# Kernel optimization log

Hardware: AMD Instinct MI355X
Metric: run time of the kernel (lower is better)

Reference implementation:

```python
import jax, jax.numpy as jnp
import numpy as np


def _chamfer(pred, target):
    # pred: [B, N, 3], target: [B, M, 3]
    # Squared euclidean pairwise distances (norm=2 in pytorch3d semantics):
    # d[b,n,m] = |p|^2 + |t|^2 - 2 p.t
    p2 = jnp.sum(pred * pred, axis=-1)      # [B, N]
    t2 = jnp.sum(target * target, axis=-1)  # [B, M]
    pt = jnp.einsum('bnd,bmd->bnm', pred, target)  # [B, N, M]
    d = p2[:, :, None] + t2[:, None, :] - 2.0 * pt  # [B, N, M]
    # bidirectional nearest-neighbor min-reduction
    cham_x = jnp.min(d, axis=2)  # [B, N] pred -> target
    cham_y = jnp.min(d, axis=1)  # [B, M] target -> pred
    # point_reduction='mean' then batch_reduction='mean' (pytorch3d defaults)
    loss = jnp.mean(jnp.mean(cham_x, axis=1) + jnp.mean(cham_y, axis=1))
    return loss


def setup_inputs() -> dict:
    key = jax.random.key(0)
    k1, k2 = jax.random.split(key)
    B, N, M, D = 16, 4096, 4096, 3
    pred = jax.random.normal(k1, (B, N, D), dtype=jnp.float32)
    target = jax.random.normal(k2, (B, M, D), dtype=jnp.float32)
    return {"pred": pred, "target": target}


def reference(pred, target):
    return _chamfer(pred, target)
```

## Files before the change

kernel.cpp:

```cpp
#include <hip/hip_runtime.h>

typedef __attribute__((ext_vector_type(8)))  short short8;
typedef __attribute__((ext_vector_type(16))) float f32x16;

#define B_SZ  16
#define NPTS  4096
#define MBLK  512
#define PRB   256
#define NCH   (NPTS / PRB)
#define STGT  512
#define STILE (STGT / 32)
#define NSTG  (NPTS / STGT)
#define NRT   (B_SZ * NPTS)

__device__ __forceinline__ unsigned short f2bf(float f) {
    unsigned u = __float_as_uint(f);
    return (unsigned short)((u + 0x7FFFu + ((u >> 16) & 1u)) >> 16);
}
__device__ __forceinline__ float bf2f(unsigned short s) {
    return __uint_as_float(((unsigned)s) << 16);
}
__device__ __forceinline__ short n2(unsigned short s) {
    return (short)f2bf(-2.0f * bf2f(s));
}

__global__ __launch_bounds__(MBLK, 2) void chamfer_fused(
    const float* __restrict__ pred, const float* __restrict__ target,
    float* __restrict__ out)
{
    __shared__ short8   sB[STILE * 64];
    __shared__ unsigned rowOut[PRB];
    __shared__ float    red[MBLK / 64];

    const int dir = blockIdx.y;
    const float* own = dir ? target : pred;
    const float* opp = dir ? pred : target;

    const int b     = blockIdx.x >> 4;
    const int chunk = blockIdx.x & (NCH - 1);
    const int tid   = threadIdx.x;
    const int lane  = tid & 63;
    const int w     = tid >> 6;
    const int r32   = lane & 31;
    const int h     = lane >> 5;
    const short ONE = (short)0x3F80;

    short8 af;
    {
        const float* pp = own +
            ((size_t)b*NPTS + chunk*PRB + w*32 + r32)*3;
        float x = pp[0], y = pp[1], z = pp[2];
        unsigned short phx=f2bf(x), phy=f2bf(y), phz=f2bf(z);
        unsigned short plx=f2bf(x-bf2f(phx)), ply=f2bf(y-bf2f(phy)),
                       plz=f2bf(z-bf2f(phz));
        short8 v;
        if (h == 0) {
            v[0]=n2(phx); v[1]=n2(phy); v[2]=n2(phz);
            v[3]=n2(plx); v[4]=n2(ply); v[5]=n2(plz);
            v[6]=n2(phx); v[7]=n2(phy);
        } else {
            float p2 = fmaf(z,z,fmaf(y,y,x*x));
            unsigned short p2h=f2bf(p2), p2l=f2bf(p2-bf2f(p2h));
            v[0]=n2(phz); v[1]=n2(plx); v[2]=n2(ply); v[3]=n2(plz);
            v[4]=(short)p2h; v[5]=(short)p2l; v[6]=ONE; v[7]=ONE;
        }
        af = v;
    }

    f32x16 zc;
    #pragma unroll
    for (int r = 0; r < 16; ++r) zc[r] = 0.0f;
    short8 mA = {0,0,0,0,0,0,0,0}, mB = {0,0,0,0,0,0,0,0};
    if (h == 0) { mA[0] = (short)f2bf((float)r32); mB[0] = ONE; }
    f32x16 pr = __builtin_amdgcn_mfma_f32_32x32x16_bf16(mA, mB, zc, 0, 0, 0);
    int lab[16];
    bool ok = true;
    #pragma unroll
    for (int r = 0; r < 16; ++r) {
        lab[r] = ((int)(pr[r] + 0.5f)) & 31;
        ok = ok && (lab[r] == ((r & 3) + 8 * (r >> 2) + 4 * h));
    }
    const bool fast = __all(ok) != 0;

    if (!fast) rowOut[tid & (PRB - 1)] = 0x7F7F7F7Fu;

    f32x16 rmin;
    #pragma unroll
    for (int r = 0; r < 16; ++r) rmin[r] = 1e30f;

    const float* oppB = opp + (size_t)b * NPTS * 3;

    for (int s = 0; s < NSTG; ++s) {
        __syncthreads();
        #pragma unroll
        for (int i = 0; i < (STILE*64)/MBLK; ++i) {
            int e  = i * MBLK + tid;
            int t  = e >> 6, l2 = e & 63;
            int cc = l2 & 31, hh = l2 >> 5;
            const float* o = oppB + (size_t)(s*STGT + t*32 + cc)*3;
            float tx=o[0], ty=o[1], tz=o[2];
            unsigned short hx=f2bf(tx), hy=f2bf(ty), hz=f2bf(tz);
            unsigned short lx=f2bf(tx-bf2f(hx)), ly=f2bf(ty-bf2f(hy)),
                           lz=f2bf(tz-bf2f(hz));
            short8 v;
            if (hh == 0) {
                v[0]=(short)hx; v[1]=(short)hy; v[2]=(short)hz;
                v[3]=(short)hx; v[4]=(short)hy; v[5]=(short)hz;
                v[6]=(short)lx; v[7]=(short)ly;
            } else {
                float t2 = fmaf(tz,tz,fmaf(ty,ty,tx*tx));
                unsigned short t2h=f2bf(t2), t2l=f2bf(t2-bf2f(t2h));
                v[0]=(short)lz; v[1]=(short)lx; v[2]=(short)ly;
                v[3]=(short)lz; v[4]=ONE; v[5]=ONE;
                v[6]=(short)t2h; v[7]=(short)t2l;
            }
            sB[e] = v;
        }
        __syncthreads();

        for (int t = 0; t < STILE; ++t) {
            short8 b0 = sB[t*64 + lane];
            f32x16 a0 = __builtin_amdgcn_mfma_f32_32x32x16_bf16(af, b0, zc, 0,0,0);
            #pragma unroll
            for (int r = 0; r < 16; ++r)
                rmin[r] = fminf(a0[r], rmin[r]);
        }
    }

    __syncthreads();
    if (fast) {
        #pragma unroll
        for (int r = 0; r < 16; ++r) {
            float v0 = rmin[r];
            v0 = fminf(v0, __shfl_xor(v0, 1, 64));
            v0 = fminf(v0, __shfl_xor(v0, 2, 64));
            v0 = fminf(v0, __shfl_xor(v0, 4, 64));
            v0 = fminf(v0, __shfl_xor(v0, 8, 64));
            v0 = fminf(v0, __shfl_xor(v0, 16, 64));
            if (r32 == 0)
                rowOut[w*32 + lab[r]] = __float_as_uint(v0);
        }
    } else {
        #pragma unroll
        for (int r = 0; r < 16; ++r)
            atomicMin(&rowOut[w*32 + lab[r]],
                      __float_as_uint(fmaxf(rmin[r], 0.0f)));
    }
    __syncthreads();

    float v = (tid < PRB) ? __uint_as_float(rowOut[tid]) : 0.0f;
    for (int off = 32; off > 0; off >>= 1)
        v += __shfl_down(v, off, 64);
    if ((tid & 63) == 0) red[w] = v;
    __syncthreads();
    if (tid == 0) {
        float s = 0.0f;
        #pragma unroll
        for (int i = 0; i < MBLK / 64; ++i) s += red[i];
        atomicAdd(out, s * (1.0f / (float)NRT));
    }
}

extern "C" void kernel_launch(void* const* d_in, const int* in_sizes, int n_in,
                              void* d_out, int out_size, void* d_ws, size_t ws_size,
                              hipStream_t stream) {
    const float* pred   = (const float*)d_in[0];
    const float* target = (const float*)d_in[1];
    float* out = (float*)d_out;

    hipMemsetAsync(out, 0, sizeof(float), stream);

    dim3 grid(B_SZ * NCH, 2);
    chamfer_fused<<<grid, MBLK, 0, stream>>>(pred, target, out);
}
```

Before: 36.09 us.

## Prefetch next target stage into registers and double stage size

```diff
diff --git a/kernel.cpp b/kernel.cpp
--- a/kernel.cpp
+++ b/kernel.cpp
@@ -8,9 +8,10 @@
 #define MBLK  512
 #define PRB   256
 #define NCH   (NPTS / PRB)
-#define STGT  512
+#define STGT  1024
 #define STILE (STGT / 32)
 #define NSTG  (NPTS / STGT)
+#define PPT   (STGT / MBLK)
 #define NRT   (B_SZ * NPTS)
 
 __device__ __forceinline__ unsigned short f2bf(float f) {
@@ -90,33 +91,45 @@
 
     const float* oppB = opp + (size_t)b * NPTS * 3;
 
+    float rx[PPT], ry[PPT], rz[PPT];
+    #pragma unroll
+    for (int j = 0; j < PPT; ++j) {
+        const float* o = oppB + (size_t)(j * MBLK + tid) * 3;
+        rx[j] = o[0]; ry[j] = o[1]; rz[j] = o[2];
+    }
+
     for (int s = 0; s < NSTG; ++s) {
         __syncthreads();
         #pragma unroll
-        for (int i = 0; i < (STILE*64)/MBLK; ++i) {
-            int e  = i * MBLK + tid;
-            int t  = e >> 6, l2 = e & 63;
-            int cc = l2 & 31, hh = l2 >> 5;
-            const float* o = oppB + (size_t)(s*STGT + t*32 + cc)*3;
-            float tx=o[0], ty=o[1], tz=o[2];
+        for (int j = 0; j < PPT; ++j) {
+            int p  = j * MBLK + tid;
+            int t  = p >> 5, cc = p & 31;
+            float tx = rx[j], ty = ry[j], tz = rz[j];
             unsigned short hx=f2bf(tx), hy=f2bf(ty), hz=f2bf(tz);
             unsigned short lx=f2bf(tx-bf2f(hx)), ly=f2bf(ty-bf2f(hy)),
                            lz=f2bf(tz-bf2f(hz));
-            short8 v;
-            if (hh == 0) {
-                v[0]=(short)hx; v[1]=(short)hy; v[2]=(short)hz;
-                v[3]=(short)hx; v[4]=(short)hy; v[5]=(short)hz;
-                v[6]=(short)lx; v[7]=(short)ly;
-            } else {
-                float t2 = fmaf(tz,tz,fmaf(ty,ty,tx*tx));
-                unsigned short t2h=f2bf(t2), t2l=f2bf(t2-bf2f(t2h));
-                v[0]=(short)lz; v[1]=(short)lx; v[2]=(short)ly;
-                v[3]=(short)lz; v[4]=ONE; v[5]=ONE;
-                v[6]=(short)t2h; v[7]=(short)t2l;
-            }
-            sB[e] = v;
+            float t2 = fmaf(tz,tz,fmaf(ty,ty,tx*tx));
+            unsigned short t2h=f2bf(t2), t2l=f2bf(t2-bf2f(t2h));
+            short8 v0, v1;
+            v0[0]=(short)hx; v0[1]=(short)hy; v0[2]=(short)hz;
+            v0[3]=(short)hx; v0[4]=(short)hy; v0[5]=(short)hz;
+            v0[6]=(short)lx; v0[7]=(short)ly;
+            v1[0]=(short)lz; v1[1]=(short)lx; v1[2]=(short)ly;
+            v1[3]=(short)lz; v1[4]=ONE; v1[5]=ONE;
+            v1[6]=(short)t2h; v1[7]=(short)t2l;
+            sB[t*64 + cc]      = v0;
+            sB[t*64 + 32 + cc] = v1;
         }
         __syncthreads();
+
+        if (s + 1 < NSTG) {
+            #pragma unroll
+            for (int j = 0; j < PPT; ++j) {
+                const float* o = oppB +
+                    (size_t)((s + 1) * STGT + j * MBLK + tid) * 3;
+                rx[j] = o[0]; ry[j] = o[1]; rz[j] = o[2];
+            }
+        }
 
         for (int t = 0; t < STILE; ++t) {
             short8 b0 = sB[t*64 + lane];
```

New measurement: 33.78 us, median of 3. 1.07x faster.
